# Performance work log

Hardware: AMD Instinct MI355X
Metric: run time of the kernel (lower is better)

The kernel has to match this reference:

```python
import jax, jax.numpy as jnp
import numpy as np

IN_F, OUT_F, NB = 4096, 4096, 8
BS = IN_F // NB  # 512


def setup_inputs() -> dict:
    key = jax.random.key(0)
    k1, k2, k3, k4 = jax.random.split(key, 4)
    weight = jax.random.normal(k1, (OUT_F, IN_F), dtype=jnp.float32) * 0.02
    bias = jax.random.normal(k2, (OUT_F,), dtype=jnp.float32) * 0.02
    x = jax.random.normal(k3, (4, 2048, IN_F), dtype=jnp.float32)
    R_blocks = jax.random.normal(k4, (NB, BS, BS), dtype=jnp.float32) * 0.1
    return {"weight": weight, "bias": bias, "x": x, "R_blocks": R_blocks, "layer_idx": 0}


def cayley_transform(A):
    # A: [nb, bs, bs]; Q = (I - A_skew) @ inv(I + A_skew + 1e-6 I)
    bs = A.shape[-1]
    I = jnp.eye(bs, dtype=A.dtype)
    A_skew = 0.5 * (A - jnp.swapaxes(A, -2, -1))
    return jnp.matmul(I - A_skew, jnp.linalg.inv(I + A_skew + 1e-6 * I))


def reference(weight, bias, x, R_blocks, layer_idx):
    R_ortho = cayley_transform(R_blocks)  # [nb, bs, bs]
    # weight @ block_diag(R) == per-block contraction on the in_features axis
    w = weight.reshape(OUT_F, NB, BS)
    tw = jnp.einsum('onb,nbc->onc', w, R_ortho).reshape(OUT_F, IN_F)
    # F.linear: x @ tw.T + bias
    out = jnp.einsum('bsi,oi->bso', x, tw) + bias
    return out
```

## Files before the change

kernel.cpp:

```cpp
#include <hip/hip_runtime.h>
#include <hip/hip_bf16.h>


typedef unsigned short u16;
typedef __attribute__((ext_vector_type(8))) __bf16 bf16x8;
typedef __attribute__((ext_vector_type(4))) float f32x4;
typedef __attribute__((ext_vector_type(8))) unsigned short u16x8;
typedef __attribute__((ext_vector_type(4))) unsigned short u16x4;

#define C0   1.000001f
#define C1Q  2.000001f
#define AS1 __attribute__((address_space(1)))
#define AS3 __attribute__((address_space(3)))

__device__ __forceinline__ u16 f2bf(float x) {
  union { float f; unsigned u; } v; v.f = x;
  return (u16)((v.u + 0x7fffu + ((v.u >> 16) & 1u)) >> 16);
}
__device__ __forceinline__ float bf2f(u16 h) {
  union { float f; unsigned u; } v; v.u = ((unsigned)h) << 16; return v.f;
}

__device__ __forceinline__ void get_coefs(float t, float* C) {
  float lam = powf(t, 0.25f);
  float a = 2.0f / (C0 * C0 + lam);
  float e = (lam - C0 * C0) / (lam + C0 * C0);
  float sq = e * e, c1 = 2.0f / (2.0f - sq);
  C[0] = a; C[1] = 2.0f * c1; C[2] = -c1 * a;
  C[3] = 2.0f * c1 * a; C[4] = -c1 * a * a;
  e = sq / (2.0f - sq); sq = e * e;
  float c2 = 2.0f / (2.0f - sq);
  C[5] = 2.0f * c2; C[6] = -c2;
  e = sq / (2.0f - sq); sq = e * e;
  float c3 = 2.0f / (2.0f - sq);
  C[7] = 2.0f * c3; C[8] = -c3;
}

__global__ __launch_bounds__(256) void k_build_M(const float* __restrict__ R,
                                                 u16* __restrict__ Mh,
                                                 u16* __restrict__ Ml) {
  __shared__ float t1[32][33];
  const int n = blockIdx.z;
  const int tr = blockIdx.y * 32, tc = blockIdx.x * 32;
  const int ly = threadIdx.x >> 5, lx = threadIdx.x & 31;
  const float* Rb = R + (size_t)n * 262144;
  float a[4];
#pragma unroll
  for (int i = 0; i < 4; ++i) {
    a[i] = Rb[(size_t)(tr + ly + i * 8) * 512 + tc + lx];
    t1[ly + i * 8][lx] = Rb[(size_t)(tc + ly + i * 8) * 512 + tr + lx];
  }
  __syncthreads();
#pragma unroll
  for (int i = 0; i < 4; ++i) {
    const int r = tr + ly + i * 8, c = tc + lx;
    float m = 0.5f * (a[i] - t1[lx][ly + i * 8]) + (r == c ? C0 : 0.0f);
    u16 h = f2bf(m);
    const size_t idx = (size_t)n * 262144 + (size_t)r * 512 + c;
    Mh[idx] = h;
    Ml[idx] = f2bf(m - bf2f(h));
  }
}

__global__ __launch_bounds__(256) void k_init(const u16* __restrict__ Mh,
                                              const u16* __restrict__ Ml,
                                              const u16* __restrict__ G,
                                              const u16* __restrict__ G2,
                                              const float* __restrict__ part,
                                              float* __restrict__ coef,
                                              u16* __restrict__ X0,
                                              u16* __restrict__ T2) {
  __shared__ float sp[64];
  __shared__ float sc[9];
  const int n = blockIdx.x >> 7;
  if (threadIdx.x < 64) sp[threadIdx.x] = part[n * 64 + threadIdx.x];
  __syncthreads();
  if (threadIdx.x == 0) {
    float s = 0.f;
    for (int i = 0; i < 64; ++i) s += sp[i];
    float C[9];
    get_coefs(s, C);
#pragma unroll
    for (int k = 0; k < 9; ++k) sc[k] = C[k];
    coef[n] = C[0];
    coef[8 + n]  = C[1]; coef[16 + n] = C[2];
    coef[24 + n] = C[3]; coef[32 + n] = C[4];
    coef[40 + n] = C[5]; coef[48 + n] = C[6];
    coef[56 + n] = C[7]; coef[64 + n] = C[8];
  }
  __syncthreads();
  const size_t base = ((size_t)blockIdx.x * 256 + threadIdx.x) * 8;
  const int r  = (int)((base >> 9) & 511);
  const int c0 = (int)(base & 511);
  u16x8 mh = *reinterpret_cast<const u16x8*>(Mh + base);
  u16x8 ml = *reinterpret_cast<const u16x8*>(Ml + base);
  u16x8 g  = *reinterpret_cast<const u16x8*>(G  + base);
  u16x8 g2 = *reinterpret_cast<const u16x8*>(G2 + base);
  u16x8 x0, t2;
#pragma unroll
  for (int e = 0; e < 8; ++e) {
    float m = bf2f(mh[e]) + bf2f(ml[e]);
    x0[e] = f2bf(sc[0] * ((r == c0 + e ? 2.0f * C0 : 0.0f) - m));
    t2[e] = f2bf(sc[3] * bf2f(g[e]) + sc[4] * bf2f(g2[e]));
  }
  *reinterpret_cast<u16x8*>(X0 + base) = x0;
  *reinterpret_cast<u16x8*>(T2 + base) = t2;
}

#define BMM_FRAGS(rs)                                                          \
  bf16x8 a[2], b[2], al2[2], bl2[2];                                           \
  _Pragma("unroll")                                                            \
  for (int i = 0; i < 2; ++i) {                                                \
    const int fr = wr * 32 + i * 16 + c15;                                     \
    const int ia = (rs) * 2048 + fr * 32 + ((lk ^ (fr & 3)) * 8);              \
    a[i] = *reinterpret_cast<const bf16x8*>(&sA[ia]);                          \
    if constexpr (PROD3) al2[i] = *reinterpret_cast<const bf16x8*>(&sAl[ia]);  \
  }                                                                            \
  _Pragma("unroll")                                                            \
  for (int j = 0; j < 2; ++j) {                                                \
    const int fc = wc * 32 + j * 16 + c15;                                     \
    const int ib = (rs) * 2048 + fc * 32 + ((lk ^ (fc & 3)) * 8);              \
    b[j] = *reinterpret_cast<const bf16x8*>(&sB[ib]);                          \
    if constexpr (PROD3) bl2[j] = *reinterpret_cast<const bf16x8*>(&sBl[ib]);  \
  }                                                                            \
  _Pragma("unroll")                                                            \
  for (int i = 0; i < 2; ++i)                                                  \
    _Pragma("unroll")                                                          \
    for (int j = 0; j < 2; ++j) {                                              \
      acc[i][j] = __builtin_amdgcn_mfma_f32_16x16x32_bf16(a[i], b[j], acc[i][j], 0, 0, 0); \
      if constexpr (PROD3) {                                                   \
        acc[i][j] = __builtin_amdgcn_mfma_f32_16x16x32_bf16(a[i],   bl2[j], acc[i][j], 0, 0, 0); \
        acc[i][j] = __builtin_amdgcn_mfma_f32_16x16x32_bf16(al2[i], b[j],   acc[i][j], 0, 0, 0); \
      }                                                                        \
    }

#define BMM_WAIT(SEL)                                                          \
  if ((SEL) == 0) {                                                            \
    if constexpr (PROD3) asm volatile("s_waitcnt vmcnt(12)" ::: "memory");     \
    else                 asm volatile("s_waitcnt vmcnt(6)" ::: "memory");      \
  } else if ((SEL) == 1) {                                                     \
    if constexpr (PROD3) asm volatile("s_waitcnt vmcnt(8)" ::: "memory");      \
    else                 asm volatile("s_waitcnt vmcnt(4)" ::: "memory");      \
  } else if ((SEL) == 2) {                                                     \
    if constexpr (PROD3) asm volatile("s_waitcnt vmcnt(4)" ::: "memory");      \
    else                 asm volatile("s_waitcnt vmcnt(2)" ::: "memory");      \
  } else {                                                                     \
    asm volatile("s_waitcnt vmcnt(0)" ::: "memory");                           \
  }

template <int PROD3, int DMODE, int OMODE, int DUAL, int FROB>
__global__ __launch_bounds__(256)
void k_bmm(const u16* __restrict__ Ah, const u16* __restrict__ Al,
           const u16* __restrict__ Bh, const u16* __restrict__ Bl,
           const u16* __restrict__ Dh, const u16* __restrict__ Dl,
           u16* __restrict__ Cnh, u16* __restrict__ Cnl,
           u16* __restrict__ Cth, u16* __restrict__ Ctl,
           float cd, float cs,
           const float* __restrict__ cdp, const float* __restrict__ csp,
           const float* __restrict__ cvsrc, u16* __restrict__ cvdst, int zmm,
           const u16* __restrict__ A2, const u16* __restrict__ B2,
           const u16* __restrict__ D2, u16* __restrict__ C2,
           float* __restrict__ part) {
  __shared__ __align__(16) u16 sA[5 * 2048], sB[5 * 2048];
  __shared__ __align__(16) u16 sAl[PROD3 ? 5 * 2048 : 8];
  __shared__ __align__(16) u16 sBl[PROD3 ? 5 * 2048 : 8];
  __shared__ float fred[FROB ? 4 : 1];

  if ((int)blockIdx.z >= zmm) {
    const int zi = ((int)blockIdx.z - zmm) * 64 + blockIdx.y * 8 + blockIdx.x;
    const int chunk = zi >> 7;
    const int base = (zi & 127) * 256 + (int)threadIdx.x;
    const float* src = cvsrc + (size_t)chunk * 4194304;
    u16* dst = cvdst + (size_t)chunk * 4194304;
#pragma unroll
    for (int e = 0; e < 16; ++e) {
      const size_t g = (size_t)(base + e * 32768) * 8;
      float4 f0 = *reinterpret_cast<const float4*>(src + g);
      float4 f1 = *reinterpret_cast<const float4*>(src + g + 4);
      u16x8 w;
      w[0] = f2bf(f0.x); w[1] = f2bf(f0.y); w[2] = f2bf(f0.z); w[3] = f2bf(f0.w);
      w[4] = f2bf(f1.x); w[5] = f2bf(f1.y); w[6] = f2bf(f1.z); w[7] = f2bf(f1.w);
      *reinterpret_cast<u16x8*>(dst + g) = w;
    }
    return;
  }

  const int zq = DUAL ? ((blockIdx.z >> 3) & 1) : 0;
  const u16* Ah_ = (DUAL && zq) ? A2 : Ah;
  const u16* Bh_ = (DUAL && zq) ? B2 : Bh;
  const u16* Dh_ = (DUAL && zq) ? D2 : Dh;
  u16* Cnh_ = (DUAL && zq) ? C2 : Cnh;
  const size_t zb = (size_t)(blockIdx.z & 7) * 262144;
  const int tid = threadIdx.x, lane = tid & 63, wave = tid >> 6;
  const int m0 = blockIdx.y * 64, n0 = blockIdx.x * 64;
  const int wr = wave >> 1, wc = wave & 1;
  const int c15 = lane & 15, lk = lane >> 4;
  const int srow = tid >> 2;
  const int sg = (tid & 3) ^ (srow & 3);
  f32x4 acc[2][2] = {};
  const u16* pa = Ah_ + zb + (size_t)(m0 + srow) * 512 + sg * 8;
  const u16* pb = Bh_ + zb + (size_t)(n0 + srow) * 512 + sg * 8;
  const u16* pal = PROD3 ? Al + zb + (size_t)(m0 + srow) * 512 + sg * 8 : pa;
  const u16* pbl = PROD3 ? Bl + zb + (size_t)(n0 + srow) * 512 + sg * 8 : pb;

  int jn = 0, js = 0;
  auto STG = [&]() {
    if (jn < 16) {
      const int off = jn << 5;
      __builtin_amdgcn_global_load_lds((const AS1 void*)(pa + off),
                                       (AS3 void*)(sA + js * 2048 + tid * 8), 16, 0, 0);
      __builtin_amdgcn_global_load_lds((const AS1 void*)(pb + off),
                                       (AS3 void*)(sB + js * 2048 + tid * 8), 16, 0, 0);
      if constexpr (PROD3) {
        __builtin_amdgcn_global_load_lds((const AS1 void*)(pal + off),
                                         (AS3 void*)(sAl + js * 2048 + tid * 8), 16, 0, 0);
        __builtin_amdgcn_global_load_lds((const AS1 void*)(pbl + off),
                                         (AS3 void*)(sBl + js * 2048 + tid * 8), 16, 0, 0);
      }
    }
    ++jn; js = (js == 4) ? 0 : js + 1;
  };

  STG(); STG(); STG();
  int rs = 0;
  for (int t = 0; t < 13; ++t) {
    STG();
    BMM_WAIT(0)
    __builtin_amdgcn_s_barrier();
    BMM_FRAGS(rs)
    rs = (rs == 4) ? 0 : rs + 1;
  }
  STG();
  BMM_WAIT(1)
  __builtin_amdgcn_s_barrier();
  { BMM_FRAGS(rs) }
  rs = (rs == 4) ? 0 : rs + 1;
  STG();
  BMM_WAIT(2)
  __builtin_amdgcn_s_barrier();
  { BMM_FRAGS(rs) }
  rs = (rs == 4) ? 0 : rs + 1;
  STG();
  BMM_WAIT(3)
  __builtin_amdgcn_s_barrier();
  { BMM_FRAGS(rs) }

  const float cdL = cdp ? cdp[blockIdx.z & 7] : cd;
  const float csL = csp ? csp[blockIdx.z & 7] : cs;
  float fs = 0.f;
#pragma unroll
  for (int i = 0; i < 2; ++i)
#pragma unroll
    for (int j = 0; j < 2; ++j) {
      const int rowb = m0 + wr * 32 + i * 16 + lk * 4;
      const int col  = n0 + wc * 32 + j * 16 + c15;
      u16 hv[4], lv[4];
#pragma unroll
      for (int r = 0; r < 4; ++r) {
        float val = csL * acc[i][j][r];
        if constexpr (DMODE >= 1) {
          float d = bf2f(Dh_[zb + (size_t)(rowb + r) * 512 + col]);
          if constexpr (DMODE == 2) d += bf2f(Dl[zb + (size_t)(rowb + r) * 512 + col]);
          val += cdL * d;
        }
        u16 h = f2bf(val);
        if constexpr (OMODE & 1) Cnh_[zb + (size_t)(rowb + r) * 512 + col] = h;
        if constexpr (FROB) { float v = bf2f(h); fs += v * v; }
        u16 l = 0;
        if constexpr (OMODE & 10) l = f2bf(val - bf2f(h));
        if constexpr (OMODE & 2) Cnl[zb + (size_t)(rowb + r) * 512 + col] = l;
        hv[r] = h; lv[r] = l;
      }
      if constexpr (OMODE & 4) {
        u16x4 v; v[0] = hv[0]; v[1] = hv[1]; v[2] = hv[2]; v[3] = hv[3];
        *reinterpret_cast<u16x4*>(&Cth[zb + (size_t)col * 512 + rowb]) = v;
      }
      if constexpr (OMODE & 8) {
        u16x4 v; v[0] = lv[0]; v[1] = lv[1]; v[2] = lv[2]; v[3] = lv[3];
        *reinterpret_cast<u16x4*>(&Ctl[zb + (size_t)col * 512 + rowb]) = v;
      }
    }
  if constexpr (FROB) {
    for (int off = 32; off; off >>= 1) fs += __shfl_down(fs, off, 64);
    if ((tid & 63) == 0) fred[tid >> 6] = fs;
    __syncthreads();
    if (tid == 0)
      part[(blockIdx.z & 7) * 64 + blockIdx.y * 8 + blockIdx.x] =
          fred[0] + fred[1] + fred[2] + fred[3];
  }
}

__global__ __launch_bounds__(256)
void k_twmm(const u16* __restrict__ W, const u16* __restrict__ Qt,
            u16* __restrict__ tw) {
  __shared__ __align__(16) u16 sA[5 * 2048], sB[5 * 2048];
  const int z = blockIdx.z;
  const size_t zb = (size_t)z * 262144;
  const int tid = threadIdx.x, lane = tid & 63, wave = tid >> 6;
  const int m0 = blockIdx.y * 64, n0 = blockIdx.x * 64;
  const int wr = wave >> 1, wc = wave & 1;
  const int c15 = lane & 15, lk = lane >> 4;
  const int srow = tid >> 2;
  const int sg = (tid & 3) ^ (srow & 3);
  f32x4 acc[2][2] = {};
  const u16* pa = W + (size_t)(m0 + srow) * 4096 + z * 512 + sg * 8;
  const u16* pb = Qt + zb + (size_t)(n0 + srow) * 512 + sg * 8;

  int jn = 0, js = 0;
  auto STG = [&]() {
    if (jn < 16) {
      const int off = jn << 5;
      __builtin_amdgcn_global_load_lds((const AS1 void*)(pa + off),
                                       (AS3 void*)(sA + js * 2048 + tid * 8), 16, 0, 0);
      __builtin_amdgcn_global_load_lds((const AS1 void*)(pb + off),
                                       (AS3 void*)(sB + js * 2048 + tid * 8), 16, 0, 0);
    }
    ++jn; js = (js == 4) ? 0 : js + 1;
  };

#define TW_FRAGS(rs)                                                           \
  {                                                                            \
    bf16x8 a[2], b[2];                                                         \
    _Pragma("unroll")                                                          \
    for (int i = 0; i < 2; ++i) {                                              \
      const int fr = wr * 32 + i * 16 + c15;                                   \
      a[i] = *reinterpret_cast<const bf16x8*>(                                 \
          &sA[(rs) * 2048 + fr * 32 + ((lk ^ (fr & 3)) * 8)]);                 \
    }                                                                          \
    _Pragma("unroll")                                                          \
    for (int j = 0; j < 2; ++j) {                                              \
      const int fc = wc * 32 + j * 16 + c15;                                   \
      b[j] = *reinterpret_cast<const bf16x8*>(                                 \
          &sB[(rs) * 2048 + fc * 32 + ((lk ^ (fc & 3)) * 8)]);                 \
    }                                                                          \
    _Pragma("unroll")                                                          \
    for (int i = 0; i < 2; ++i)                                                \
      _Pragma("unroll")                                                        \
      for (int j = 0; j < 2; ++j)                                              \
        acc[i][j] = __builtin_amdgcn_mfma_f32_16x16x32_bf16(a[i], b[j], acc[i][j], 0, 0, 0); \
  }

  STG(); STG(); STG();
  int rs = 0;
  for (int t = 0; t < 13; ++t) {
    STG();
    asm volatile("s_waitcnt vmcnt(6)" ::: "memory");
    __builtin_amdgcn_s_barrier();
    TW_FRAGS(rs)
    rs = (rs == 4) ? 0 : rs + 1;
  }
  STG();
  asm volatile("s_waitcnt vmcnt(4)" ::: "memory");
  __builtin_amdgcn_s_barrier();
  TW_FRAGS(rs)
  rs = (rs == 4) ? 0 : rs + 1;
  STG();
  asm volatile("s_waitcnt vmcnt(2)" ::: "memory");
  __builtin_amdgcn_s_barrier();
  TW_FRAGS(rs)
  rs = (rs == 4) ? 0 : rs + 1;
  STG();
  asm volatile("s_waitcnt vmcnt(0)" ::: "memory");
  __builtin_amdgcn_s_barrier();
  TW_FRAGS(rs)

#pragma unroll
  for (int i = 0; i < 2; ++i)
#pragma unroll
    for (int j = 0; j < 2; ++j) {
      const int rowb = m0 + wr * 32 + i * 16 + lk * 4;
      const int col  = z * 512 + n0 + wc * 32 + j * 16 + c15;
#pragma unroll
      for (int r = 0; r < 4; ++r)
        tw[(size_t)(rowb + r) * 4096 + col] = f2bf(acc[i][j][r]);
    }
}

#define NSL 18

#define RD_A3(dst, MH)                                                         \
  _Pragma("unroll")                                                            \
  for (int m = 0; m < 4; ++m)                                                  \
    dst[m] = *reinterpret_cast<const bf16x8*>(                                 \
        &lds[aslot * 4096 + ((MH) * 64 + m * 16 + c15) * 32 + gsw * 8]);

#define RD_B3(dst)                                                             \
  _Pragma("unroll")                                                            \
  for (int n = 0; n < 4; ++n)                                                  \
    dst[n] = *reinterpret_cast<const bf16x8*>(                                 \
        &lds[bslot * 4096 + (bq64 + n * 16 + c15) * 32 + gsw * 8]);

#define MFMA16(afX, bfX, MH)                                                   \
  __builtin_amdgcn_s_setprio(1);                                               \
  _Pragma("unroll")                                                            \
  for (int m = 0; m < 4; ++m)                                                  \
    _Pragma("unroll")                                                          \
    for (int n = 0; n < 4; ++n)                                                \
      acc[(MH) * 4 + m][n] = __builtin_amdgcn_mfma_f32_16x16x32_bf16(          \
          afX[m], bfX[n], acc[(MH) * 4 + m][n], 0, 0, 0);                      \
  __builtin_amdgcn_s_setprio(0);

#define TILE32(WM)                                                             \
  {                                                                            \
    int aslot = s0 + wr;            if (aslot >= NSL) aslot -= NSL;            \
    int bslot = s0 + 2 + (wc >> 1); if (bslot >= NSL) bslot -= NSL;            \
    STAGE(); STAGE();                                                          \
    RD_B3(bfr)                                                                 \
    RD_A3(afA, 0)                                                              \
    MFMA16(afA, bfr, 0)                                                        \
    STAGE(); STAGE();                                                          \
    RD_A3(afB, 1)                                                              \
    MFMA16(afB, bfr, 1)                                                        \
    if ((WM) == 1) asm volatile("s_waitcnt vmcnt(8)" ::: "memory");            \
    if ((WM) == 2) asm volatile("s_waitcnt vmcnt(4)" ::: "memory");            \
    if ((WM) == 3) asm volatile("s_waitcnt vmcnt(0)" ::: "memory");            \
    if ((WM) != 0) {                                                           \
      __builtin_amdgcn_s_barrier();                                            \
      __builtin_amdgcn_sched_barrier(0);                                       \
    }                                                                          \
    s0 += 4; if (s0 >= NSL) s0 -= NSL;                                         \
  }

__global__ __launch_bounds__(512, 2)
void k_gemm256(const u16* __restrict__ A, const u16* __restrict__ B,
               const float* __restrict__ bias,
               float* __restrict__ C, int N, int K) {
  __shared__ __align__(16) u16 lds[NSL * 4096];
  const int tid = threadIdx.x, lane = tid & 63, wave = tid >> 6;
  int bid = blockIdx.y * gridDim.x + blockIdx.x;
  const int cpx = (gridDim.x * gridDim.y) >> 3;
  bid = (bid & 7) * cpx + (bid >> 3);
  const int nbx = N >> 8;
  const int bx = bid % nbx, by = bid / nbx;
  const int m0 = by << 8, n0 = bx << 8;
  const int wr = wave >> 2, wc = wave & 3;
  const int srow = tid >> 2;
  const int sgc  = (tid & 3) ^ ((srow >> 1) & 3);
  const int c15 = lane & 15, lq = lane >> 4;
  const int gsw = lq ^ ((c15 >> 1) & 3);
  const int bq64 = (wc & 1) * 64;
  const int NT = K >> 5;

  f32x4 acc[8][4] = {};
  bf16x8 afA[4], afB[4], bfr[4];

  int jn = 0, js = 0;
  auto STAGE = [&]() {
    if (jn < 4 * NT) {
      const int t = jn >> 2, q = jn & 3;
      const u16* srcb = (q < 2)
          ? A + (size_t)(m0 + q * 128 + srow) * (size_t)K
          : B + (size_t)(n0 + (q - 2) * 128 + srow) * (size_t)K;
      const u16* src = srcb + (t << 5) + sgc * 8;
      u16* dst = (u16*)lds + js * 4096 + tid * 8;
      __builtin_amdgcn_global_load_lds(
          (const AS1 void*)src, (AS3 void*)dst, 16, 0, 0);
    }
    ++jn; js = (js == NSL - 1) ? 0 : js + 1;
  };

#pragma unroll
  for (int i = 0; i < 12; ++i) STAGE();
  asm volatile("s_waitcnt vmcnt(8)" ::: "memory");
  __builtin_amdgcn_s_barrier();
  __builtin_amdgcn_sched_barrier(0);

  int s0 = 0;
  for (int tau = 0; tau < NT - 3; ++tau) {
    TILE32(1)
  }
  TILE32(2)
  TILE32(3)
  TILE32(0)

#pragma unroll
  for (int n = 0; n < 4; ++n) {
    const int col = n0 + wc * 64 + n * 16 + c15;
    const float bv = bias[col];
#pragma unroll
    for (int mi = 0; mi < 8; ++mi) {
      const int rowb = m0 + wr * 128 + mi * 16 + (lq << 2);
#pragma unroll
      for (int r = 0; r < 4; ++r)
        C[(size_t)(rowb + r) * N + col] = acc[mi][n][r] + bv;
    }
  }
}

extern "C" void kernel_launch(void* const* d_in, const int* in_sizes, int n_in,
                              void* d_out, int out_size, void* d_ws, size_t ws_size,
                              hipStream_t stream) {
  const float* W    = (const float*)d_in[0];
  const float* bias = (const float*)d_in[1];
  const float* x    = (const float*)d_in[2];
  const float* R    = (const float*)d_in[3];
  float* out = (float*)d_out;

  char* ws = (char*)d_ws;
  u16* x_bf = (u16*)(ws);
  u16* tw   = (u16*)(ws + 67108864);
  u16* W_bf = (u16*)(ws + 100663296);

  char* arena = (char*)d_out;
  auto slot = [&](int i) -> u16* { return (u16*)(arena + (size_t)i * 4194304); };
  u16 *Mh = slot(0), *Ml = slot(1);
  u16 *G = slot(2), *G2 = slot(3);
  u16 *X0 = slot(5), *T2 = slot(6), *X1 = slot(7), *X2 = slot(8), *T3 = slot(9);
  u16 *X3h = slot(10), *X3l = slot(11), *X3th = slot(12), *X3tl = slot(13);
  u16 *Tpth = slot(14), *Tptl = slot(15);
  u16 *X4h = slot(16), *X4l = slot(17), *X4th = slot(18), *X4tl = slot(19);
  u16 *Qt = slot(20);
  float* coef = (float*)(arena + (size_t)21 * 4194304);
  float* part = coef + 1024;

  const u16* NUL = nullptr;
  const float* NULF = nullptr;
  u16* NULW = nullptr;
  float* NULP = nullptr;
  const dim3 gC0(8, 8, 8);
  const dim3 gC2(8, 8, 12);

  k_build_M<<<dim3(16, 16, 8), 256, 0, stream>>>(R, Mh, Ml);
  k_bmm<0, 0, 1, 0, 0><<<gC2, 256, 0, stream>>>(Mh, NUL, Mh, NUL, NUL, NUL,
      G, NULW, NULW, NULW, 0.f, 1.f, NULF, NULF, W, W_bf, 8,
      NUL, NUL, NUL, NULW, NULP);
  k_bmm<0, 0, 1, 0, 1><<<gC2, 256, 0, stream>>>(G, NUL, G, NUL, NUL, NUL,
      G2, NULW, NULW, NULW, 0.f, 1.f, NULF, NULF,
      W + (size_t)2 * 4194304, W_bf + (size_t)2 * 4194304, 8,
      NUL, NUL, NUL, NULW, part);
  k_init<<<1024, 256, 0, stream>>>(Mh, Ml, G, G2, part, coef, X0, T2);
  k_bmm<0, 1, 1, 0, 0><<<gC2, 256, 0, stream>>>(X0, NUL, G, NUL, X0, NUL,
      X1, NULW, NULW, NULW, 0.f, 0.f, coef + 8, coef + 16,
      x, x_bf, 8, NUL, NUL, NUL, NULW, NULP);
  k_bmm<0, 1, 1, 1, 0><<<dim3(8, 8, 20), 256, 0, stream>>>(X1, NUL, T2, NUL, X1, NUL,
      X2, NULW, NULW, NULW, 0.f, 0.f, coef + 40, coef + 48,
      x + (size_t)2 * 4194304, x_bf + (size_t)2 * 4194304, 16,
      T2, T2, T2, T3, NULP);
  k_bmm<0, 1, 15, 0, 0><<<gC2, 256, 0, stream>>>(X2, NUL, T3, NUL, X2, NUL,
      X3h, X3l, X3th, X3tl, 0.f, 0.f, coef + 56, coef + 64,
      x + (size_t)4 * 4194304, x_bf + (size_t)4 * 4194304, 8,
      NUL, NUL, NUL, NULW, NULP);
  k_bmm<1, 0, 12, 0, 0><<<gC2, 256, 0, stream>>>(Mh, Ml, X3th, X3tl, NUL, NUL,
      NULW, NULW, Tpth, Tptl, 0.f, 1.f, NULF, NULF,
      x + (size_t)6 * 4194304, x_bf + (size_t)6 * 4194304, 8,
      NUL, NUL, NUL, NULW, NULP);
  k_bmm<1, 2, 15, 0, 0><<<gC0, 256, 0, stream>>>(X3h, X3l, Tpth, Tptl, X3h, X3l,
      X4h, X4l, X4th, X4tl, 2.f, -1.f, NULF, NULF,
      x, x_bf, 8, NUL, NUL, NUL, NULW, NULP);
  k_bmm<1, 2, 4, 0, 0><<<gC0, 256, 0, stream>>>(Mh, Ml, X4th, X4tl, X4h, X4l,
      NULW, NULW, Qt, NULW, C1Q, -1.f, NULF, NULF,
      x, x_bf, 8, NUL, NUL, NUL, NULW, NULP);
  k_twmm<<<dim3(8, 64, 8), 256, 0, stream>>>(W_bf, Qt, tw);
  k_gemm256<<<dim3(16, 32), 512, 0, stream>>>(x_bf, tw, bias, out, 4096, 4096);
}
```

Before: 487.6 us.

## Restructure Newton-Schulz inverse chain to drop two batched matmul launches

```diff
diff --git a/kernel.cpp b/kernel.cpp
--- a/kernel.cpp
+++ b/kernel.cpp
@@ -66,12 +66,13 @@
                                               const u16* __restrict__ Ml,
                                               const u16* __restrict__ G,
                                               const u16* __restrict__ G2,
+                                              const u16* __restrict__ H,
                                               const float* __restrict__ part,
                                               float* __restrict__ coef,
-                                              u16* __restrict__ X0,
+                                              u16* __restrict__ X1,
                                               u16* __restrict__ T2) {
   __shared__ float sp[64];
-  __shared__ float sc[9];
+  __shared__ float sc[13];
   const int n = blockIdx.x >> 7;
   if (threadIdx.x < 64) sp[threadIdx.x] = part[n * 64 + threadIdx.x];
   __syncthreads();
@@ -82,6 +83,10 @@
     get_coefs(s, C);
 #pragma unroll
     for (int k = 0; k < 9; ++k) sc[k] = C[k];
+    sc[9]  = 2.0f * C0 * C[3];
+    sc[10] = -C[3];
+    sc[11] = 2.0f * C0 * C[4];
+    sc[12] = -C[4];
     coef[n] = C[0];
     coef[8 + n]  = C[1]; coef[16 + n] = C[2];
     coef[24 + n] = C[3]; coef[32 + n] = C[4];
@@ -96,14 +101,17 @@
   u16x8 ml = *reinterpret_cast<const u16x8*>(Ml + base);
   u16x8 g  = *reinterpret_cast<const u16x8*>(G  + base);
   u16x8 g2 = *reinterpret_cast<const u16x8*>(G2 + base);
-  u16x8 x0, t2;
+  u16x8 hh = *reinterpret_cast<const u16x8*>(H  + base);
+  u16x8 x1, t2;
 #pragma unroll
   for (int e = 0; e < 8; ++e) {
     float m = bf2f(mh[e]) + bf2f(ml[e]);
-    x0[e] = f2bf(sc[0] * ((r == c0 + e ? 2.0f * C0 : 0.0f) - m));
-    t2[e] = f2bf(sc[3] * bf2f(g[e]) + sc[4] * bf2f(g2[e]));
-  }
-  *reinterpret_cast<u16x8*>(X0 + base) = x0;
+    float gv = bf2f(g[e]);
+    x1[e] = f2bf((r == c0 + e ? sc[9] : 0.0f) + sc[10] * m + sc[11] * gv +
+                 sc[12] * bf2f(hh[e]));
+    t2[e] = f2bf(sc[3] * gv + sc[4] * bf2f(g2[e]));
+  }
+  *reinterpret_cast<u16x8*>(X1 + base) = x1;
   *reinterpret_cast<u16x8*>(T2 + base) = t2;
 }
 
@@ -148,7 +156,7 @@
     asm volatile("s_waitcnt vmcnt(0)" ::: "memory");                           \
   }
 
-template <int PROD3, int DMODE, int OMODE, int DUAL, int FROB>
+template <int PROD3, int DMODE, int OMODE, int DUAL, int FROB, int VOUT = 0>
 __global__ __launch_bounds__(256)
 void k_bmm(const u16* __restrict__ Ah, const u16* __restrict__ Al,
            const u16* __restrict__ Bh, const u16* __restrict__ Bl,
@@ -258,18 +266,24 @@
 #pragma unroll
       for (int r = 0; r < 4; ++r) {
         float val = csL * acc[i][j][r];
+        float dv = 0.f;
         if constexpr (DMODE >= 1) {
-          float d = bf2f(Dh_[zb + (size_t)(rowb + r) * 512 + col]);
-          if constexpr (DMODE == 2) d += bf2f(Dl[zb + (size_t)(rowb + r) * 512 + col]);
-          val += cdL * d;
+          dv = bf2f(Dh_[zb + (size_t)(rowb + r) * 512 + col]);
+          if constexpr (DMODE == 2) dv += bf2f(Dl[zb + (size_t)(rowb + r) * 512 + col]);
         }
-        u16 h = f2bf(val);
-        if constexpr (OMODE & 1) Cnh_[zb + (size_t)(rowb + r) * 512 + col] = h;
-        if constexpr (FROB) { float v = bf2f(h); fs += v * v; }
-        u16 l = 0;
-        if constexpr (OMODE & 10) l = f2bf(val - bf2f(h));
-        if constexpr (OMODE & 2) Cnl[zb + (size_t)(rowb + r) * 512 + col] = l;
-        hv[r] = h; lv[r] = l;
+        float nval, tval;
+        if constexpr (VOUT) { tval = val; nval = cdL * dv - val; }
+        else { nval = tval = val + cdL * dv; }
+        u16 nh = f2bf(nval);
+        if constexpr (OMODE & 1) Cnh_[zb + (size_t)(rowb + r) * 512 + col] = nh;
+        if constexpr (FROB) { float v = bf2f(nh); fs += v * v; }
+        if constexpr (OMODE & 2)
+          Cnl[zb + (size_t)(rowb + r) * 512 + col] = f2bf(nval - bf2f(nh));
+        if constexpr (OMODE & 12) {
+          u16 th = f2bf(tval);
+          hv[r] = th;
+          if constexpr (OMODE & 8) lv[r] = f2bf(tval - bf2f(th));
+        }
       }
       if constexpr (OMODE & 4) {
         u16x4 v; v[0] = hv[0]; v[1] = hv[1]; v[2] = hv[2]; v[3] = hv[3];
@@ -284,7 +298,7 @@
     for (int off = 32; off; off >>= 1) fs += __shfl_down(fs, off, 64);
     if ((tid & 63) == 0) fred[tid >> 6] = fs;
     __syncthreads();
-    if (tid == 0)
+    if (tid == 0 && (int)blockIdx.z < 8)
       part[(blockIdx.z & 7) * 64 + blockIdx.y * 8 + blockIdx.x] =
           fred[0] + fred[1] + fred[2] + fred[3];
   }
@@ -504,11 +518,11 @@
   char* arena = (char*)d_out;
   auto slot = [&](int i) -> u16* { return (u16*)(arena + (size_t)i * 4194304); };
   u16 *Mh = slot(0), *Ml = slot(1);
-  u16 *G = slot(2), *G2 = slot(3);
-  u16 *X0 = slot(5), *T2 = slot(6), *X1 = slot(7), *X2 = slot(8), *T3 = slot(9);
+  u16 *G = slot(2), *G2 = slot(3), *H = slot(4);
+  u16 *T2 = slot(6), *X1 = slot(7), *X2 = slot(8), *T3 = slot(9);
   u16 *X3h = slot(10), *X3l = slot(11), *X3th = slot(12), *X3tl = slot(13);
   u16 *Tpth = slot(14), *Tptl = slot(15);
-  u16 *X4h = slot(16), *X4l = slot(17), *X4th = slot(18), *X4tl = slot(19);
+  u16 *Vh = slot(16), *Vl = slot(17);
   u16 *Qt = slot(20);
   float* coef = (float*)(arena + (size_t)21 * 4194304);
   float* part = coef + 1024;
@@ -517,39 +531,33 @@
   const float* NULF = nullptr;
   u16* NULW = nullptr;
   float* NULP = nullptr;
-  const dim3 gC0(8, 8, 8);
   const dim3 gC2(8, 8, 12);
+  const dim3 gD2(8, 8, 20);
 
   k_build_M<<<dim3(16, 16, 8), 256, 0, stream>>>(R, Mh, Ml);
   k_bmm<0, 0, 1, 0, 0><<<gC2, 256, 0, stream>>>(Mh, NUL, Mh, NUL, NUL, NUL,
       G, NULW, NULW, NULW, 0.f, 1.f, NULF, NULF, W, W_bf, 8,
       NUL, NUL, NUL, NULW, NULP);
-  k_bmm<0, 0, 1, 0, 1><<<gC2, 256, 0, stream>>>(G, NUL, G, NUL, NUL, NUL,
+  k_bmm<0, 0, 1, 1, 1><<<gD2, 256, 0, stream>>>(G, NUL, G, NUL, NUL, NUL,
       G2, NULW, NULW, NULW, 0.f, 1.f, NULF, NULF,
-      W + (size_t)2 * 4194304, W_bf + (size_t)2 * 4194304, 8,
-      NUL, NUL, NUL, NULW, part);
-  k_init<<<1024, 256, 0, stream>>>(Mh, Ml, G, G2, part, coef, X0, T2);
-  k_bmm<0, 1, 1, 0, 0><<<gC2, 256, 0, stream>>>(X0, NUL, G, NUL, X0, NUL,
-      X1, NULW, NULW, NULW, 0.f, 0.f, coef + 8, coef + 16,
-      x, x_bf, 8, NUL, NUL, NUL, NULW, NULP);
-  k_bmm<0, 1, 1, 1, 0><<<dim3(8, 8, 20), 256, 0, stream>>>(X1, NUL, T2, NUL, X1, NUL,
+      W + (size_t)2 * 4194304, W_bf + (size_t)2 * 4194304, 16,
+      Mh, G, NUL, H, part);
+  k_init<<<1024, 256, 0, stream>>>(Mh, Ml, G, G2, H, part, coef, X1, T2);
+  k_bmm<0, 1, 1, 1, 0><<<gD2, 256, 0, stream>>>(X1, NUL, T2, NUL, X1, NUL,
       X2, NULW, NULW, NULW, 0.f, 0.f, coef + 40, coef + 48,
-      x + (size_t)2 * 4194304, x_bf + (size_t)2 * 4194304, 16,
-      T2, T2, T2, T3, NULP);
+      x, x_bf, 16, T2, T2, T2, T3, NULP);
   k_bmm<0, 1, 15, 0, 0><<<gC2, 256, 0, stream>>>(X2, NUL, T3, NUL, X2, NUL,
       X3h, X3l, X3th, X3tl, 0.f, 0.f, coef + 56, coef + 64,
+      x + (size_t)2 * 4194304, x_bf + (size_t)2 * 4194304, 8,
+      NUL, NUL, NUL, NULW, NULP);
+  k_bmm<1, 2, 15, 0, 0, 1><<<gC2, 256, 0, stream>>>(Mh, Ml, X3th, X3tl,
+      X3h, X3l, Vh, Vl, Tpth, Tptl, C1Q, 1.f, NULF, NULF,
       x + (size_t)4 * 4194304, x_bf + (size_t)4 * 4194304, 8,
       NUL, NUL, NUL, NULW, NULP);
-  k_bmm<1, 0, 12, 0, 0><<<gC2, 256, 0, stream>>>(Mh, Ml, X3th, X3tl, NUL, NUL,
-      NULW, NULW, Tpth, Tptl, 0.f, 1.f, NULF, NULF,
+  k_bmm<1, 2, 4, 0, 0><<<gC2, 256, 0, stream>>>(Vh, Vl, Tpth, Tptl, Vh, Vl,
+      NULW, NULW, Qt, NULW, 2.f, -1.f, NULF, NULF,
       x + (size_t)6 * 4194304, x_bf + (size_t)6 * 4194304, 8,
       NUL, NUL, NUL, NULW, NULP);
-  k_bmm<1, 2, 15, 0, 0><<<gC0, 256, 0, stream>>>(X3h, X3l, Tpth, Tptl, X3h, X3l,
-      X4h, X4l, X4th, X4tl, 2.f, -1.f, NULF, NULF,
-      x, x_bf, 8, NUL, NUL, NUL, NULW, NULP);
-  k_bmm<1, 2, 4, 0, 0><<<gC0, 256, 0, stream>>>(Mh, Ml, X4th, X4tl, X4h, X4l,
-      NULW, NULW, Qt, NULW, C1Q, -1.f, NULF, NULF,
-      x, x_bf, 8, NUL, NUL, NUL, NULW, NULP);
   k_twmm<<<dim3(8, 64, 8), 256, 0, stream>>>(W_bf, Qt, tw);
   k_gemm256<<<dim3(16, 32), 512, 0, stream>>>(x_bf, tw, bias, out, 4096, 4096);
 }
```

New measurement: 467.8 us (median of 3 runs). 1.04x faster.
